# Kernel optimization log

Measured on AMD Instinct MI355X. Metric: run time of the kernel, lower is better.

Reference implementation:

```python
import jax, jax.numpy as jnp
import numpy as np

B, T_DEC, F = 16, 32, 8
S_ENC, H, L = 256, 512, 2
TGT_IDX = jnp.arange(8)  # target_indices = all features


def setup_inputs() -> dict:
    key = jax.random.key(0)
    ks = jax.random.split(key, 16)
    g = lambda k, shp, s=0.05: jax.random.normal(k, shp, dtype=jnp.float32) * s
    return {
        'target': jax.random.normal(ks[0], (B, T_DEC, F), dtype=jnp.float32),
        'hidden0': jax.random.normal(ks[1], (L, B, H), dtype=jnp.float32),
        'enc_outputs': jax.random.normal(ks[2], (B, S_ENC, H), dtype=jnp.float32),
        # Attention params
        'attn_W': g(ks[3], (H, 2 * H)), 'attn_b': jnp.zeros((H,), jnp.float32),
        'v_w': g(ks[4], (H,)),
        # GRU layer 0 (input = F + H) and layer 1 (input = H); PyTorch layout [3H, in]
        'gru_Wih0': g(ks[5], (3 * H, F + H)), 'gru_Whh0': g(ks[6], (3 * H, H)),
        'gru_bih0': jnp.zeros((3 * H,), jnp.float32), 'gru_bhh0': jnp.zeros((3 * H,), jnp.float32),
        'gru_Wih1': g(ks[7], (3 * H, H)), 'gru_Whh1': g(ks[8], (3 * H, H)),
        'gru_bih1': jnp.zeros((3 * H,), jnp.float32), 'gru_bhh1': jnp.zeros((3 * H,), jnp.float32),
        # output Linear (2H + F -> F)
        'out_W': g(ks[9], (F, 2 * H + F)), 'out_b': jnp.zeros((F,), jnp.float32),
        'input_seq_len': S_ENC,
    }


def _gru_cell(x, h, Wih, Whh, bih, bhh):
    # PyTorch GRUCell math; gate order [r, z, n]
    gi = x @ Wih.T + bih
    gh = h @ Whh.T + bhh
    ir, iz, inn = jnp.split(gi, 3, axis=-1)
    hr, hz, hn = jnp.split(gh, 3, axis=-1)
    r = jax.nn.sigmoid(ir + hr)
    z = jax.nn.sigmoid(iz + hz)
    n = jnp.tanh(inn + r * hn)
    return (1.0 - z) * n + z * h


def reference(target, hidden0, enc_outputs, attn_W, attn_b, v_w,
              gru_Wih0, gru_Whh0, gru_bih0, gru_bhh0,
              gru_Wih1, gru_Whh1, gru_bih1, gru_bhh1,
              out_W, out_b, input_seq_len):
    b, s, h = enc_outputs.shape

    def step(carry, target_t):
        hidden, x_in = carry  # hidden [L,B,H], x_in [B,F]
        h_top = hidden[-1]
        # Bahdanau attention
        hid_rep = jnp.broadcast_to(h_top[:, None, :], (b, s, h))
        energy = jnp.tanh(jnp.concatenate([hid_rep, enc_outputs], axis=-1) @ attn_W.T + attn_b)
        scores = energy @ v_w  # [B,S]
        weightings = jax.nn.softmax(scores, axis=1)
        weighted = jnp.einsum('bs,bsh->bh', weightings, enc_outputs)  # [B,H]
        # stacked GRU single step
        x = jnp.concatenate([x_in, weighted], axis=-1)  # [B, F+H]
        h0 = _gru_cell(x, hidden[0], gru_Wih0, gru_Whh0, gru_bih0, gru_bhh0)
        h1 = _gru_cell(h0, hidden[1], gru_Wih1, gru_Whh1, gru_bih1, gru_bhh1)
        new_hidden = jnp.stack([h0, h1])
        # output projection + relu (applied in DecoderBase.forward)
        out = jnp.concatenate([h1, weighted, x_in], axis=-1) @ out_W.T + out_b
        out = jax.nn.relu(out)  # [B,F]
        # no teacher forcing (teacher_force_prob=None): replace target features with prediction
        next_in = target_t.at[:, TGT_IDX].set(out)
        return (new_hidden, next_in), out

    target_ts = jnp.swapaxes(target, 0, 1)  # [T,B,F]
    (_, _), outs = jax.lax.scan(step, (hidden0, target[:, 0, :]), target_ts)
    return jnp.swapaxes(outs, 0, 1)  # [B,T,F]
```

## Files before the change

### kernel.cpp

```cpp
#include <hip/hip_runtime.h>


namespace {
constexpr int NBLK = 256, NTHR = 256;


constexpr int OFF_AEH   = 8192;
constexpr int OFF_WHID  = OFF_AEH + 131072;
constexpr int OFF_WIH0  = OFF_WHID + 131072;
constexpr int OFF_WHH0  = OFF_WIH0 + 399360;
constexpr int OFF_WIH1  = OFF_WHH0 + 393216;
constexpr int OFF_WHH1  = OFF_WIH1 + 393216;
constexpr int OFF_ENCP  = OFF_WHH1 + 393216;
constexpr int OFF_H0C   = OFF_ENCP + 1048576;
constexpr int OFF_H1C   = OFF_H0C + 4096;
constexpr int OFF_HIDPS = OFF_H1C + 4096;
constexpr int OFF_WPART = OFF_HIDPS + 8192;
constexpr int OFF_H0S   = OFF_WPART + 135168;
constexpr int OFF_H1S   = OFF_H0S + 4096;

constexpr int L_H1   = 0;
constexpr int L_H0   = 256;
constexpr int L_HIDP = 512;
constexpr int L_ES   = 1024;
constexpr int L_HX   = 1040;
constexpr int L_AX   = 1304;
constexpr int L_AH   = 1400;
constexpr int L_BIH0 = 1496, L_BHH0 = 1592, L_BIH1 = 1688, L_BHH1 = 1784;
constexpr int L_VW   = 1880;
constexpr int L_XINL = 2392;
constexpr int LDS_FLOATS = 8192;
}

typedef _Float16 h2 __attribute__((ext_vector_type(2)));
union U32H { unsigned u; h2 h; };

__device__ __forceinline__ float dot2(unsigned a, unsigned b, float acc) {
    U32H ua, ub; ua.u = a; ub.u = b;
#if __has_builtin(__builtin_amdgcn_fdot2)
    return __builtin_amdgcn_fdot2(ua.h, ub.h, acc, false);
#else
    return acc + (float)ua.h.x * (float)ub.h.x + (float)ua.h.y * (float)ub.h.y;
#endif
}
__device__ __forceinline__ unsigned packh2(float a, float b) {
    U32H u; u.h = h2{(_Float16)a, (_Float16)b}; return u.u;
}
__device__ __forceinline__ float fsig(float x) { return 1.0f / (1.0f + __expf(-x)); }
__device__ __forceinline__ float ftanhf(float x) {
    float e = __expf(2.0f * x);
    return 1.0f - 2.0f / (e + 1.0f);
}
__device__ __forceinline__ float cload(const float* p) {
    return __hip_atomic_load(p, __ATOMIC_RELAXED, __HIP_MEMORY_SCOPE_SYSTEM);
}
__device__ __forceinline__ void cstore(float* p, float v) {
    __hip_atomic_store(p, v, __ATOMIC_RELAXED, __HIP_MEMORY_SCOPE_SYSTEM);
}
__device__ __forceinline__ unsigned ucload(const unsigned* p) {
    return __hip_atomic_load(p, __ATOMIC_RELAXED, __HIP_MEMORY_SCOPE_SYSTEM);
}
__device__ __forceinline__ void ucstore(unsigned* p, unsigned v) {
    __hip_atomic_store(p, v, __ATOMIC_RELAXED, __HIP_MEMORY_SCOPE_SYSTEM);
}

__device__ __forceinline__ void bar_sync_flush(unsigned* cnt, unsigned target) {
    __syncthreads();
    if (threadIdx.x == 0) {
        __builtin_amdgcn_fence(__ATOMIC_RELEASE, "agent");
        __hip_atomic_fetch_add(cnt, 1u, __ATOMIC_RELAXED, __HIP_MEMORY_SCOPE_SYSTEM);
        while (__hip_atomic_load(cnt, __ATOMIC_RELAXED, __HIP_MEMORY_SCOPE_SYSTEM) < target)
            __builtin_amdgcn_s_sleep(8);
        __builtin_amdgcn_fence(__ATOMIC_ACQUIRE, "agent");
    }
    __syncthreads();
}

__global__ __launch_bounds__(NTHR) void decoder_kernel(
    const float* __restrict__ target, const float* __restrict__ hidden0,
    const float* __restrict__ enc, const float* __restrict__ attn_W,
    const float* __restrict__ attn_b, const float* __restrict__ v_w,
    const float* __restrict__ Wih0, const float* __restrict__ Whh0,
    const float* __restrict__ bih0, const float* __restrict__ bhh0,
    const float* __restrict__ Wih1, const float* __restrict__ Whh1,
    const float* __restrict__ bih1, const float* __restrict__ bhh1,
    const float* __restrict__ outW, const float* __restrict__ outBias,
    float* __restrict__ out, float* __restrict__ ws) {
    const int tid = threadIdx.x, bid = blockIdx.x;
    const int b = bid >> 4, s = bid & 15;
    unsigned* tags = (unsigned*)ws;
    unsigned* gridCnt = (unsigned*)ws + 8180;

    unsigned* aehU  = (unsigned*)(ws + OFF_AEH);
    unsigned* whidU = (unsigned*)(ws + OFF_WHID);
    unsigned* wih0U = (unsigned*)(ws + OFF_WIH0);
    unsigned* whh0U = (unsigned*)(ws + OFF_WHH0);
    unsigned* wih1U = (unsigned*)(ws + OFF_WIH1);
    unsigned* whh1U = (unsigned*)(ws + OFF_WHH1);
    unsigned* encpU = (unsigned*)(ws + OFF_ENCP);
    unsigned* h0cU = (unsigned*)(ws + OFF_H0C);
    unsigned* h1cU = (unsigned*)(ws + OFF_H1C);
    float* hidPS = ws + OFF_HIDPS;
    float* wpart = ws + OFF_WPART;
    unsigned* h0S = (unsigned*)(ws + OFF_H0S);
    unsigned* h1S = (unsigned*)(ws + OFF_H1S);

    __shared__ __align__(16) float lds[LDS_FLOATS];
    unsigned* ldsU = (unsigned*)lds;
    const int gtid = bid * NTHR + tid;

    for (int i = gtid; i < 131072; i += NBLK * NTHR) {
        const int jr = i >> 8, p = i & 255;
        aehU[i]  = packh2(attn_W[jr * 1024 + 512 + 2 * p], attn_W[jr * 1024 + 513 + 2 * p]);
        whidU[i] = packh2(attn_W[jr * 1024 + 2 * p], attn_W[jr * 1024 + 1 + 2 * p]);
    }
    for (int i = gtid; i < 399360; i += NBLK * NTHR)
        wih0U[i] = packh2(Wih0[2 * i], Wih0[2 * i + 1]);
    for (int i = gtid; i < 393216; i += NBLK * NTHR) {
        whh0U[i] = packh2(Whh0[2 * i], Whh0[2 * i + 1]);
        wih1U[i] = packh2(Wih1[2 * i], Wih1[2 * i + 1]);
        whh1U[i] = packh2(Whh1[2 * i], Whh1[2 * i + 1]);
    }
    if (gtid < 4096) {
        const int bb = gtid >> 8, p = gtid & 255;
        h0cU[gtid] = packh2(hidden0[bb * 512 + 2 * p], hidden0[bb * 512 + 2 * p + 1]);
        h1cU[gtid] = packh2(hidden0[8192 + bb * 512 + 2 * p], hidden0[8192 + bb * 512 + 2 * p + 1]);
    }
    bar_sync_flush(gridCnt, NBLK);

    {
        for (int i = 0; i < 32; ++i) {
            const int idx = tid + i * 256;
            lds[idx] = enc[(b * 256 + s * 16) * 512 + idx];
        }
        __syncthreads();
        float a0[16], a1[16];
        const float bb0 = attn_b[2 * tid], bb1 = attn_b[2 * tid + 1];
#pragma unroll
        for (int sl = 0; sl < 16; ++sl) { a0[sl] = bb0; a1[sl] = bb1; }
        const unsigned* w0 = &aehU[(2 * tid) * 256];
        const unsigned* w1 = &aehU[(2 * tid + 1) * 256];
        for (int p = 0; p < 256; ++p) {
            const unsigned ww0 = w0[p], ww1 = w1[p];
#pragma unroll
            for (int sl = 0; sl < 16; ++sl) {
                const unsigned epk = packh2(lds[sl * 512 + 2 * p], lds[sl * 512 + 2 * p + 1]);
                a0[sl] = dot2(epk, ww0, a0[sl]);
                a1[sl] = dot2(epk, ww1, a1[sl]);
            }
        }
        for (int sl = 0; sl < 16; ++sl)
            encpU[(b * 256 + s * 16 + sl) * 256 + tid] = packh2(a0[sl], a1[sl]);
        __syncthreads();
    }

    if (tid < 96) {
        const int grow = (tid >> 5) * 512 + s * 32 + (tid & 31);
        lds[L_BIH0 + tid] = bih0[grow]; lds[L_BHH0 + tid] = bhh0[grow];
        lds[L_BIH1 + tid] = bih1[grow]; lds[L_BHH1 + tid] = bhh1[grow];
    }
    lds[L_VW + tid] = v_w[tid];
    lds[L_VW + 256 + tid] = v_w[256 + tid];
    __syncthreads();

    ldsU[L_H1 + tid] = ucload(&h1cU[b * 256 + tid]);
    ldsU[L_H0 + tid] = ucload(&h0cU[b * 256 + tid]);
    if (tid < 8) lds[L_XINL + tid] = target[b * 256 + tid];
    __syncthreads();

    for (int t = 0; t < 32; ++t) {
        const unsigned tgt = (unsigned)(t + 1);

        {
            const int r = tid >> 3, sub = tid & 7;
            const uint4* wrow = (const uint4*)&whidU[(s * 32 + r) * 256 + sub * 32];
            const uint4* h1p = (const uint4*)&ldsU[L_H1 + sub * 32];
            float acc = 0.f;
#pragma unroll
            for (int k4 = 0; k4 < 8; ++k4) {
                const uint4 hv = h1p[k4], wv = wrow[k4];
                acc = dot2(hv.x, wv.x, acc); acc = dot2(hv.y, wv.y, acc);
                acc = dot2(hv.z, wv.z, acc); acc = dot2(hv.w, wv.w, acc);
            }
            acc += __shfl_down(acc, 4, 8); acc += __shfl_down(acc, 2, 8); acc += __shfl_down(acc, 1, 8);
            if (sub == 0) cstore(&hidPS[(b * 16 + s) * 32 + r], acc);
        }
        __syncthreads();
        if (tid == 0) ucstore(&tags[(b * 16 + s) * 32 + 0], tgt);
        {
            const unsigned* tg = &tags[(b * 16 + (tid & 15)) * 32 + 0];
            while (ucload(tg) < tgt) __builtin_amdgcn_s_sleep(1);
        }
        __builtin_amdgcn_fence(__ATOMIC_ACQUIRE, "workgroup");
        lds[L_HIDP + tid] = cload(&hidPS[(b * 16 + (tid >> 5)) * 32 + (tid & 31)]);
        lds[L_HIDP + 256 + tid] = cload(&hidPS[(b * 16 + 8 + (tid >> 5)) * 32 + (tid & 31)]);
        __syncthreads();

        {
            const int sloc = tid >> 4, sub = tid & 15;
            const unsigned* ep = &encpU[(b * 256 + s * 16 + sloc) * 256];
            float acc = 0.f;
#pragma unroll 4
            for (int k2 = 0; k2 < 16; ++k2) {
                const int p = k2 * 16 + sub;
                U32H u; u.u = ep[p];
                acc += lds[L_VW + 2 * p] * ftanhf((float)u.h.x + lds[L_HIDP + 2 * p]);
                acc += lds[L_VW + 2 * p + 1] * ftanhf((float)u.h.y + lds[L_HIDP + 2 * p + 1]);
            }
            acc += __shfl_down(acc, 8, 16); acc += __shfl_down(acc, 4, 16);
            acc += __shfl_down(acc, 2, 16); acc += __shfl_down(acc, 1, 16);
            if (sub == 0) lds[L_ES + sloc] = __expf(acc);
        }
        __syncthreads();
        {
            float wp0 = 0.f, wp1 = 0.f;
            const float2* er = (const float2*)&enc[(b * 256 + s * 16) * 512];
#pragma unroll
            for (int sl = 0; sl < 16; ++sl) {
                const float2 e = er[sl * 256 + tid];
                const float es = lds[L_ES + sl];
                wp0 += es * e.x; wp1 += es * e.y;
            }
            cstore(&wpart[(b * 16 + s) * 528 + 2 * tid], wp0);
            cstore(&wpart[(b * 16 + s) * 528 + 2 * tid + 1], wp1);
            if (tid == 0) {
                float l = 0.f;
#pragma unroll
                for (int i = 0; i < 16; ++i) l += lds[L_ES + i];
                cstore(&wpart[(b * 16 + s) * 528 + 512], l);
            }
        }
        __syncthreads();
        if (tid == 0) ucstore(&tags[(b * 16 + s) * 32 + 1], tgt);
        {
            const unsigned* tg = &tags[(b * 16 + (tid & 15)) * 32 + 1];
            while (ucload(tg) < tgt) __builtin_amdgcn_s_sleep(1);
        }
        __builtin_amdgcn_fence(__ATOMIC_ACQUIRE, "workgroup");
        {
            float w0 = 0.f, w1 = 0.f;
#pragma unroll
            for (int sp = 0; sp < 16; ++sp) {
                w0 += cload(&wpart[(b * 16 + sp) * 528 + 2 * tid]);
                w1 += cload(&wpart[(b * 16 + sp) * 528 + 2 * tid + 1]);
            }
            if (tid < 16) lds[L_ES + tid] = cload(&wpart[(b * 16 + tid) * 528 + 512]);
            __syncthreads();
            float L = 0.f;
#pragma unroll
            for (int i = 0; i < 16; ++i) L += lds[L_ES + i];
            const float inv = 1.f / L;
            ldsU[L_HX + 4 + tid] = packh2(w0 * inv, w1 * inv);
            if (tid < 4) {
                ldsU[L_HX + tid] = packh2(lds[L_XINL + 2 * tid], lds[L_XINL + 2 * tid + 1]);
                ldsU[L_HX + 260 + tid] = 0u;
            }
        }
        __syncthreads();

        if (tid < 192) {
            const int u = tid >> 1, sub = tid & 1;
            const int gh = u >> 5, r = u & 31;
            const int grow = gh * 512 + s * 32 + r;
            const uint4* wx = (const uint4*)&wih0U[grow * 260 + sub * 132];
            const uint4* xp = (const uint4*)&ldsU[L_HX + sub * 132];
            float ax = 0.f;
#pragma unroll 11
            for (int k4 = 0; k4 < 33; ++k4) {
                const uint4 xv = xp[k4], wv = wx[k4];
                ax = dot2(xv.x, wv.x, ax); ax = dot2(xv.y, wv.y, ax);
                ax = dot2(xv.z, wv.z, ax); ax = dot2(xv.w, wv.w, ax);
            }
            const uint4* wh = (const uint4*)&whh0U[grow * 256 + sub * 128];
            const uint4* hp = (const uint4*)&ldsU[L_H0 + sub * 128];
            float ah = 0.f;
#pragma unroll 8
            for (int k4 = 0; k4 < 32; ++k4) {
                const uint4 hv = hp[k4], wv = wh[k4];
                ah = dot2(hv.x, wv.x, ah); ah = dot2(hv.y, wv.y, ah);
                ah = dot2(hv.z, wv.z, ah); ah = dot2(hv.w, wv.w, ah);
            }
            ax += __shfl_down(ax, 1, 2); ah += __shfl_down(ah, 1, 2);
            if (sub == 0) {
                lds[L_AX + u] = ax + lds[L_BIH0 + u];
                lds[L_AH + u] = ah + lds[L_BHH0 + u];
            }
        }
        __syncthreads();
        if (tid < 32) {
            const int r = tid;
            const float rg = fsig(lds[L_AX + r] + lds[L_AH + r]);
            const float z = fsig(lds[L_AX + 32 + r] + lds[L_AH + 32 + r]);
            const float n = ftanhf(lds[L_AX + 64 + r] + rg * lds[L_AH + 64 + r]);
            U32H u; u.u = ldsU[L_H0 + s * 16 + (r >> 1)];
            const float hold = (r & 1) ? (float)u.h.y : (float)u.h.x;
            const float hs = (1.f - z) * n + z * hold;
            const float hsn = __shfl_down(hs, 1, 2);
            if ((r & 1) == 0)
                ucstore(&h0S[(b * 16 + s) * 16 + (r >> 1)], packh2(hs, hsn));
        }
        __syncthreads();
        if (tid == 0) ucstore(&tags[(b * 16 + s) * 32 + 2], tgt);
        {
            const unsigned* tg = &tags[(b * 16 + (tid & 15)) * 32 + 2];
            while (ucload(tg) < tgt) __builtin_amdgcn_s_sleep(1);
        }
        __builtin_amdgcn_fence(__ATOMIC_ACQUIRE, "workgroup");
        ldsU[L_H0 + tid] = ucload(&h0S[(b * 16 + (tid >> 4)) * 16 + (tid & 15)]);
        __syncthreads();

        if (tid < 192) {
            const int u = tid >> 1, sub = tid & 1;
            const int gh = u >> 5, r = u & 31;
            const int grow = gh * 512 + s * 32 + r;
            const uint4* wx = (const uint4*)&wih1U[grow * 256 + sub * 128];
            const uint4* xp = (const uint4*)&ldsU[L_H0 + sub * 128];
            float ax = 0.f;
#pragma unroll 8
            for (int k4 = 0; k4 < 32; ++k4) {
                const uint4 xv = xp[k4], wv = wx[k4];
                ax = dot2(xv.x, wv.x, ax); ax = dot2(xv.y, wv.y, ax);
                ax = dot2(xv.z, wv.z, ax); ax = dot2(xv.w, wv.w, ax);
            }
            const uint4* wh = (const uint4*)&whh1U[grow * 256 + sub * 128];
            const uint4* hp = (const uint4*)&ldsU[L_H1 + sub * 128];
            float ah = 0.f;
#pragma unroll 8
            for (int k4 = 0; k4 < 32; ++k4) {
                const uint4 hv = hp[k4], wv = wh[k4];
                ah = dot2(hv.x, wv.x, ah); ah = dot2(hv.y, wv.y, ah);
                ah = dot2(hv.z, wv.z, ah); ah = dot2(hv.w, wv.w, ah);
            }
            ax += __shfl_down(ax, 1, 2); ah += __shfl_down(ah, 1, 2);
            if (sub == 0) {
                lds[L_AX + u] = ax + lds[L_BIH1 + u];
                lds[L_AH + u] = ah + lds[L_BHH1 + u];
            }
        }
        __syncthreads();
        if (tid < 32) {
            const int r = tid;
            const float rg = fsig(lds[L_AX + r] + lds[L_AH + r]);
            const float z = fsig(lds[L_AX + 32 + r] + lds[L_AH + 32 + r]);
            const float n = ftanhf(lds[L_AX + 64 + r] + rg * lds[L_AH + 64 + r]);
            U32H u; u.u = ldsU[L_H1 + s * 16 + (r >> 1)];
            const float hold = (r & 1) ? (float)u.h.y : (float)u.h.x;
            const float hs = (1.f - z) * n + z * hold;
            const float hsn = __shfl_down(hs, 1, 2);
            if ((r & 1) == 0)
                ucstore(&h1S[(b * 16 + s) * 16 + (r >> 1)], packh2(hs, hsn));
        }
        __syncthreads();
        if (tid == 0) ucstore(&tags[(b * 16 + s) * 32 + 3], tgt);
        {
            const unsigned* tg = &tags[(b * 16 + (tid & 15)) * 32 + 3];
            while (ucload(tg) < tgt) __builtin_amdgcn_s_sleep(1);
        }
        __builtin_amdgcn_fence(__ATOMIC_ACQUIRE, "workgroup");
        ldsU[L_H1 + tid] = ucload(&h1S[(b * 16 + (tid >> 4)) * 16 + (tid & 15)]);
        __syncthreads();

        {
            const int f = tid >> 5, l = tid & 31;
            const float* ow = &outW[f * 1032];
            float acc = 0.f;
#pragma unroll
            for (int i = 0; i < 8; ++i) {
                const int k2 = i * 32 + l;
                U32H u; u.u = ldsU[L_H1 + k2];
                acc += ow[2 * k2] * (float)u.h.x + ow[2 * k2 + 1] * (float)u.h.y;
            }
#pragma unroll
            for (int i = 0; i < 8; ++i) {
                const int k2 = i * 32 + l;
                U32H u; u.u = ldsU[L_HX + 4 + k2];
                acc += ow[512 + 2 * k2] * (float)u.h.x + ow[512 + 2 * k2 + 1] * (float)u.h.y;
            }
            if (l < 8) acc += ow[1024 + l] * lds[L_XINL + l];
            acc += __shfl_down(acc, 16, 32); acc += __shfl_down(acc, 8, 32);
            acc += __shfl_down(acc, 4, 32); acc += __shfl_down(acc, 2, 32);
            acc += __shfl_down(acc, 1, 32);
            if (l == 0) {
                const float o = fmaxf(acc + outBias[f], 0.f);
                lds[L_ES + f] = o;
                if (s == 0) out[b * 256 + t * 8 + f] = o;
            }
        }
        __syncthreads();
        if (tid < 8) lds[L_XINL + tid] = lds[L_ES + tid];
        __syncthreads();
    }
}

extern "C" void kernel_launch(void* const* d_in, const int* in_sizes, int n_in,
                              void* d_out, int out_size, void* d_ws, size_t ws_size,
                              hipStream_t stream) {
    (void)in_sizes; (void)n_in; (void)out_size; (void)ws_size;
    hipMemsetAsync(d_ws, 0, 32768, stream);
    decoder_kernel<<<NBLK, NTHR, 0, stream>>>(
        (const float*)d_in[0], (const float*)d_in[1], (const float*)d_in[2],
        (const float*)d_in[3], (const float*)d_in[4], (const float*)d_in[5],
        (const float*)d_in[6], (const float*)d_in[7], (const float*)d_in[8],
        (const float*)d_in[9], (const float*)d_in[10], (const float*)d_in[11],
        (const float*)d_in[12], (const float*)d_in[13], (const float*)d_in[14],
        (const float*)d_in[15], (float*)d_out, (float*)d_ws);
}
```

Measured before the change: 896.0 us.

## Split prologue into separate kernels and use stamped LL messages for inter-block exchange

Moves the weight packing and encoder projection into separate kernel launches, which removes the in-kernel grid barrier and reduces the decoder's LDS footprint. Three of the four per-step flag-then-data exchanges between the 16 blocks of a batch row are replaced by 64-bit stores that carry the payload together with a step stamp, so consumers poll the data directly instead of waiting on a separate tag. The attention partial exchange still uses a flag, but now one wave signals per 64 threads after a vmcnt wait rather than going through a block-wide barrier. This trades extra launches and a larger memset for fewer barrier round trips on the serial 32-step critical path, and it relies on the inline-asm sc0/sc1 coherence being correct.

Measured after the change: 1.040 ms. +16.0%, slower.

```diff
diff --git a/kernel.cpp b/kernel.cpp
--- a/kernel.cpp
+++ b/kernel.cpp
@@ -2,22 +2,21 @@
 
 
 namespace {
-constexpr int NBLK = 256, NTHR = 256;
-
-
-constexpr int OFF_AEH   = 8192;
-constexpr int OFF_WHID  = OFF_AEH + 131072;
-constexpr int OFF_WIH0  = OFF_WHID + 131072;
-constexpr int OFF_WHH0  = OFF_WIH0 + 399360;
-constexpr int OFF_WIH1  = OFF_WHH0 + 393216;
-constexpr int OFF_WHH1  = OFF_WIH1 + 393216;
-constexpr int OFF_ENCP  = OFF_WHH1 + 393216;
-constexpr int OFF_H0C   = OFF_ENCP + 1048576;
-constexpr int OFF_H1C   = OFF_H0C + 4096;
-constexpr int OFF_HIDPS = OFF_H1C + 4096;
-constexpr int OFF_WPART = OFF_HIDPS + 8192;
-constexpr int OFF_H0S   = OFF_WPART + 135168;
-constexpr int OFF_H1S   = OFF_H0S + 4096;
+constexpr int NTHR_P = 256, NBLK_P = 256;
+constexpr int NTHR = 256, NBLK = 256;
+
+constexpr int OFF_FLG     = 0;
+constexpr int OFF_HIDP_LL = 4096;
+constexpr int OFF_H0LL    = 20480;
+constexpr int OFF_H1LL    = 28672;
+constexpr int OFF_ATTP    = 36864;
+constexpr int OFF_AEH     = 168448;
+constexpr int OFF_WHID    = OFF_AEH + 131072;
+constexpr int OFF_WIH0    = OFF_WHID + 131072;
+constexpr int OFF_WHH0    = OFF_WIH0 + 399360;
+constexpr int OFF_WIH1    = OFF_WHH0 + 393216;
+constexpr int OFF_WHH1    = OFF_WIH1 + 393216;
+constexpr int OFF_ENCP    = OFF_WHH1 + 393216;
 
 constexpr int L_H1   = 0;
 constexpr int L_H0   = 256;
@@ -26,10 +25,11 @@
 constexpr int L_HX   = 1040;
 constexpr int L_AX   = 1304;
 constexpr int L_AH   = 1400;
-constexpr int L_BIH0 = 1496, L_BHH0 = 1592, L_BIH1 = 1688, L_BHH1 = 1784;
-constexpr int L_VW   = 1880;
-constexpr int L_XINL = 2392;
-constexpr int LDS_FLOATS = 8192;
+constexpr int L_HS   = 1496;
+constexpr int L_BIH0 = 1528, L_BHH0 = 1624, L_BIH1 = 1720, L_BHH1 = 1816;
+constexpr int L_VW   = 1912;
+constexpr int L_XIN  = 2424;
+constexpr int LDS_FLOATS = 2432;
 }
 
 typedef _Float16 h2 __attribute__((ext_vector_type(2)));
@@ -60,99 +60,110 @@
 __device__ __forceinline__ unsigned ucload(const unsigned* p) {
     return __hip_atomic_load(p, __ATOMIC_RELAXED, __HIP_MEMORY_SCOPE_SYSTEM);
 }
-__device__ __forceinline__ void ucstore(unsigned* p, unsigned v) {
-    __hip_atomic_store(p, v, __ATOMIC_RELAXED, __HIP_MEMORY_SCOPE_SYSTEM);
-}
-
-__device__ __forceinline__ void bar_sync_flush(unsigned* cnt, unsigned target) {
-    __syncthreads();
-    if (threadIdx.x == 0) {
-        __builtin_amdgcn_fence(__ATOMIC_RELEASE, "agent");
-        __hip_atomic_fetch_add(cnt, 1u, __ATOMIC_RELAXED, __HIP_MEMORY_SCOPE_SYSTEM);
-        while (__hip_atomic_load(cnt, __ATOMIC_RELAXED, __HIP_MEMORY_SCOPE_SYSTEM) < target)
-            __builtin_amdgcn_s_sleep(8);
-        __builtin_amdgcn_fence(__ATOMIC_ACQUIRE, "agent");
-    }
-    __syncthreads();
-}
-
-__global__ __launch_bounds__(NTHR) void decoder_kernel(
-    const float* __restrict__ target, const float* __restrict__ hidden0,
-    const float* __restrict__ enc, const float* __restrict__ attn_W,
-    const float* __restrict__ attn_b, const float* __restrict__ v_w,
-    const float* __restrict__ Wih0, const float* __restrict__ Whh0,
-    const float* __restrict__ bih0, const float* __restrict__ bhh0,
-    const float* __restrict__ Wih1, const float* __restrict__ Whh1,
-    const float* __restrict__ bih1, const float* __restrict__ bhh1,
-    const float* __restrict__ outW, const float* __restrict__ outBias,
-    float* __restrict__ out, float* __restrict__ ws) {
-    const int tid = threadIdx.x, bid = blockIdx.x;
-    const int b = bid >> 4, s = bid & 15;
-    unsigned* tags = (unsigned*)ws;
-    unsigned* gridCnt = (unsigned*)ws + 8180;
-
+
+__device__ __forceinline__ void ll_store(unsigned long long* p, unsigned payload,
+                                         unsigned stamp) {
+    unsigned long long v = (unsigned long long)payload | ((unsigned long long)stamp << 32);
+    asm volatile("global_store_dwordx2 %0, %1, off sc0 sc1" :: "v"(p), "v"(v) : "memory");
+}
+__device__ __forceinline__ unsigned long long ll_load(const unsigned long long* p) {
+    unsigned long long v;
+    asm volatile("global_load_dwordx2 %0, %1, off sc0 sc1\n\ts_waitcnt vmcnt(0)"
+                 : "=v"(v) : "v"(p) : "memory");
+    return v;
+}
+__device__ __forceinline__ unsigned ll_poll(const unsigned long long* p, unsigned stamp) {
+    for (;;) {
+        unsigned long long v = ll_load(p);
+        if ((unsigned)(v >> 32) == stamp) return (unsigned)v;
+        __builtin_amdgcn_s_sleep(1);
+    }
+}
+__device__ __forceinline__ void flag_store(unsigned* p, unsigned v) {
+    asm volatile("global_store_dword %0, %1, off sc0 sc1" :: "v"(p), "v"(v) : "memory");
+}
+
+__global__ __launch_bounds__(NTHR_P) void pack_kernel(
+    const float* __restrict__ attn_W, const float* __restrict__ Wih0,
+    const float* __restrict__ Whh0, const float* __restrict__ Wih1,
+    const float* __restrict__ Whh1, float* __restrict__ ws) {
     unsigned* aehU  = (unsigned*)(ws + OFF_AEH);
     unsigned* whidU = (unsigned*)(ws + OFF_WHID);
     unsigned* wih0U = (unsigned*)(ws + OFF_WIH0);
     unsigned* whh0U = (unsigned*)(ws + OFF_WHH0);
     unsigned* wih1U = (unsigned*)(ws + OFF_WIH1);
     unsigned* whh1U = (unsigned*)(ws + OFF_WHH1);
-    unsigned* encpU = (unsigned*)(ws + OFF_ENCP);
-    unsigned* h0cU = (unsigned*)(ws + OFF_H0C);
-    unsigned* h1cU = (unsigned*)(ws + OFF_H1C);
-    float* hidPS = ws + OFF_HIDPS;
-    float* wpart = ws + OFF_WPART;
-    unsigned* h0S = (unsigned*)(ws + OFF_H0S);
-    unsigned* h1S = (unsigned*)(ws + OFF_H1S);
-
-    __shared__ __align__(16) float lds[LDS_FLOATS];
-    unsigned* ldsU = (unsigned*)lds;
-    const int gtid = bid * NTHR + tid;
-
-    for (int i = gtid; i < 131072; i += NBLK * NTHR) {
+    const int gtid = blockIdx.x * NTHR_P + threadIdx.x;
+    for (int i = gtid; i < 131072; i += NBLK_P * NTHR_P) {
         const int jr = i >> 8, p = i & 255;
         aehU[i]  = packh2(attn_W[jr * 1024 + 512 + 2 * p], attn_W[jr * 1024 + 513 + 2 * p]);
         whidU[i] = packh2(attn_W[jr * 1024 + 2 * p], attn_W[jr * 1024 + 1 + 2 * p]);
     }
-    for (int i = gtid; i < 399360; i += NBLK * NTHR)
+    for (int i = gtid; i < 399360; i += NBLK_P * NTHR_P)
         wih0U[i] = packh2(Wih0[2 * i], Wih0[2 * i + 1]);
-    for (int i = gtid; i < 393216; i += NBLK * NTHR) {
+    for (int i = gtid; i < 393216; i += NBLK_P * NTHR_P) {
         whh0U[i] = packh2(Whh0[2 * i], Whh0[2 * i + 1]);
         wih1U[i] = packh2(Wih1[2 * i], Wih1[2 * i + 1]);
         whh1U[i] = packh2(Whh1[2 * i], Whh1[2 * i + 1]);
     }
-    if (gtid < 4096) {
-        const int bb = gtid >> 8, p = gtid & 255;
-        h0cU[gtid] = packh2(hidden0[bb * 512 + 2 * p], hidden0[bb * 512 + 2 * p + 1]);
-        h1cU[gtid] = packh2(hidden0[8192 + bb * 512 + 2 * p], hidden0[8192 + bb * 512 + 2 * p + 1]);
-    }
-    bar_sync_flush(gridCnt, NBLK);
-
-    {
-        for (int i = 0; i < 32; ++i) {
-            const int idx = tid + i * 256;
-            lds[idx] = enc[(b * 256 + s * 16) * 512 + idx];
-        }
-        __syncthreads();
-        float a0[16], a1[16];
-        const float bb0 = attn_b[2 * tid], bb1 = attn_b[2 * tid + 1];
-#pragma unroll
-        for (int sl = 0; sl < 16; ++sl) { a0[sl] = bb0; a1[sl] = bb1; }
-        const unsigned* w0 = &aehU[(2 * tid) * 256];
-        const unsigned* w1 = &aehU[(2 * tid + 1) * 256];
-        for (int p = 0; p < 256; ++p) {
-            const unsigned ww0 = w0[p], ww1 = w1[p];
-#pragma unroll
-            for (int sl = 0; sl < 16; ++sl) {
-                const unsigned epk = packh2(lds[sl * 512 + 2 * p], lds[sl * 512 + 2 * p + 1]);
-                a0[sl] = dot2(epk, ww0, a0[sl]);
-                a1[sl] = dot2(epk, ww1, a1[sl]);
-            }
-        }
-        for (int sl = 0; sl < 16; ++sl)
-            encpU[(b * 256 + s * 16 + sl) * 256 + tid] = packh2(a0[sl], a1[sl]);
-        __syncthreads();
-    }
+}
+
+__global__ __launch_bounds__(NTHR_P) void encp_kernel(
+    const float* __restrict__ enc, const float* __restrict__ attn_b,
+    float* __restrict__ ws) {
+    const int tid = threadIdx.x, bid = blockIdx.x;
+    const int b = bid >> 4, s = bid & 15;
+    const unsigned* aehU = (const unsigned*)(ws + OFF_AEH);
+    unsigned* encpU = (unsigned*)(ws + OFF_ENCP);
+    __shared__ __align__(16) float lds[8192];
+    for (int i = 0; i < 32; ++i) {
+        const int idx = tid + i * 256;
+        lds[idx] = enc[(b * 256 + s * 16) * 512 + idx];
+    }
+    __syncthreads();
+    float a0[16], a1[16];
+    const float bb0 = attn_b[2 * tid], bb1 = attn_b[2 * tid + 1];
+#pragma unroll
+    for (int sl = 0; sl < 16; ++sl) { a0[sl] = bb0; a1[sl] = bb1; }
+    const unsigned* w0 = &aehU[(2 * tid) * 256];
+    const unsigned* w1 = &aehU[(2 * tid + 1) * 256];
+    for (int p = 0; p < 256; ++p) {
+        const unsigned ww0 = w0[p], ww1 = w1[p];
+#pragma unroll
+        for (int sl = 0; sl < 16; ++sl) {
+            const unsigned epk = packh2(lds[sl * 512 + 2 * p], lds[sl * 512 + 2 * p + 1]);
+            a0[sl] = dot2(epk, ww0, a0[sl]);
+            a1[sl] = dot2(epk, ww1, a1[sl]);
+        }
+    }
+    for (int sl = 0; sl < 16; ++sl)
+        encpU[(b * 256 + s * 16 + sl) * 256 + tid] = packh2(a0[sl], a1[sl]);
+}
+
+__global__ __launch_bounds__(NTHR) void decoder_kernel(
+    const float* __restrict__ target, const float* __restrict__ hidden0,
+    const float* __restrict__ enc, const float* __restrict__ v_w,
+    const float* __restrict__ bih0, const float* __restrict__ bhh0,
+    const float* __restrict__ bih1, const float* __restrict__ bhh1,
+    const float* __restrict__ outW, const float* __restrict__ outBias,
+    float* __restrict__ out, float* __restrict__ ws) {
+    const int tid = threadIdx.x, bid = blockIdx.x;
+    const int b = bid >> 4, s = bid & 15;
+
+    unsigned* flg = (unsigned*)ws + OFF_FLG;
+    unsigned long long* hidpLL = (unsigned long long*)(ws + OFF_HIDP_LL);
+    unsigned long long* h0LL = (unsigned long long*)(ws + OFF_H0LL);
+    unsigned long long* h1LL = (unsigned long long*)(ws + OFF_H1LL);
+    float* attP = ws + OFF_ATTP;
+    const unsigned* whidU = (const unsigned*)(ws + OFF_WHID);
+    const unsigned* wih0U = (const unsigned*)(ws + OFF_WIH0);
+    const unsigned* whh0U = (const unsigned*)(ws + OFF_WHH0);
+    const unsigned* wih1U = (const unsigned*)(ws + OFF_WIH1);
+    const unsigned* whh1U = (const unsigned*)(ws + OFF_WHH1);
+    const unsigned* encpU = (const unsigned*)(ws + OFF_ENCP);
+
+    __shared__ __align__(16) float lds[LDS_FLOATS];
+    unsigned* ldsU = (unsigned*)lds;
 
     if (tid < 96) {
         const int grow = (tid >> 5) * 512 + s * 32 + (tid & 31);
@@ -161,11 +172,11 @@
     }
     lds[L_VW + tid] = v_w[tid];
     lds[L_VW + 256 + tid] = v_w[256 + tid];
-    __syncthreads();
-
-    ldsU[L_H1 + tid] = ucload(&h1cU[b * 256 + tid]);
-    ldsU[L_H0 + tid] = ucload(&h0cU[b * 256 + tid]);
-    if (tid < 8) lds[L_XINL + tid] = target[b * 256 + tid];
+    ldsU[L_H0 + tid] = packh2(hidden0[b * 512 + 2 * tid], hidden0[b * 512 + 2 * tid + 1]);
+    ldsU[L_H1 + tid] = packh2(hidden0[8192 + b * 512 + 2 * tid],
+                              hidden0[8192 + b * 512 + 2 * tid + 1]);
+    if (tid < 8) lds[L_XIN + tid] = target[b * 256 + tid];
+    if (tid < 4) ldsU[L_HX + 260 + tid] = 0u;
     __syncthreads();
 
     for (int t = 0; t < 32; ++t) {
@@ -183,17 +194,10 @@
                 acc = dot2(hv.z, wv.z, acc); acc = dot2(hv.w, wv.w, acc);
             }
             acc += __shfl_down(acc, 4, 8); acc += __shfl_down(acc, 2, 8); acc += __shfl_down(acc, 1, 8);
-            if (sub == 0) cstore(&hidPS[(b * 16 + s) * 32 + r], acc);
-        }
-        __syncthreads();
-        if (tid == 0) ucstore(&tags[(b * 16 + s) * 32 + 0], tgt);
-        {
-            const unsigned* tg = &tags[(b * 16 + (tid & 15)) * 32 + 0];
-            while (ucload(tg) < tgt) __builtin_amdgcn_s_sleep(1);
-        }
-        __builtin_amdgcn_fence(__ATOMIC_ACQUIRE, "workgroup");
-        lds[L_HIDP + tid] = cload(&hidPS[(b * 16 + (tid >> 5)) * 32 + (tid & 31)]);
-        lds[L_HIDP + 256 + tid] = cload(&hidPS[(b * 16 + 8 + (tid >> 5)) * 32 + (tid & 31)]);
+            if (sub == 0) ll_store(&hidpLL[b * 512 + s * 32 + r], __float_as_uint(acc), tgt);
+        }
+        lds[L_HIDP + tid] = __uint_as_float(ll_poll(&hidpLL[b * 512 + tid], tgt));
+        lds[L_HIDP + 256 + tid] = __uint_as_float(ll_poll(&hidpLL[b * 512 + 256 + tid], tgt));
         __syncthreads();
 
         {
@@ -221,30 +225,32 @@
                 const float es = lds[L_ES + sl];
                 wp0 += es * e.x; wp1 += es * e.y;
             }
-            cstore(&wpart[(b * 16 + s) * 528 + 2 * tid], wp0);
-            cstore(&wpart[(b * 16 + s) * 528 + 2 * tid + 1], wp1);
+            cstore(&attP[(b * 16 + s) * 514 + 2 * tid], wp0);
+            cstore(&attP[(b * 16 + s) * 514 + 2 * tid + 1], wp1);
             if (tid == 0) {
                 float l = 0.f;
 #pragma unroll
                 for (int i = 0; i < 16; ++i) l += lds[L_ES + i];
-                cstore(&wpart[(b * 16 + s) * 528 + 512], l);
-            }
-        }
-        __syncthreads();
-        if (tid == 0) ucstore(&tags[(b * 16 + s) * 32 + 1], tgt);
-        {
-            const unsigned* tg = &tags[(b * 16 + (tid & 15)) * 32 + 1];
-            while (ucload(tg) < tgt) __builtin_amdgcn_s_sleep(1);
-        }
+                cstore(&attP[(b * 16 + s) * 514 + 512], l);
+            }
+        }
+        asm volatile("s_waitcnt vmcnt(0)" ::: "memory");
+        if ((tid & 63) == 0)
+            flag_store(&flg[(b * 16 + s) * 16 + (tid >> 6) * 4], tgt);
+
+        if (tid < 64) {
+            const unsigned* fp = &flg[(b * 16 + (tid >> 2)) * 16 + (tid & 3) * 4];
+            while (ucload(fp) < tgt) __builtin_amdgcn_s_sleep(1);
+        }
+        __syncthreads();
         __builtin_amdgcn_fence(__ATOMIC_ACQUIRE, "workgroup");
         {
             float w0 = 0.f, w1 = 0.f;
-#pragma unroll
             for (int sp = 0; sp < 16; ++sp) {
-                w0 += cload(&wpart[(b * 16 + sp) * 528 + 2 * tid]);
-                w1 += cload(&wpart[(b * 16 + sp) * 528 + 2 * tid + 1]);
-            }
-            if (tid < 16) lds[L_ES + tid] = cload(&wpart[(b * 16 + tid) * 528 + 512]);
+                w0 += cload(&attP[(b * 16 + sp) * 514 + 2 * tid]);
+                w1 += cload(&attP[(b * 16 + sp) * 514 + 2 * tid + 1]);
+            }
+            if (tid < 16) lds[L_ES + tid] = cload(&attP[(b * 16 + tid) * 514 + 512]);
             __syncthreads();
             float L = 0.f;
 #pragma unroll
@@ -252,8 +258,7 @@
             const float inv = 1.f / L;
             ldsU[L_HX + 4 + tid] = packh2(w0 * inv, w1 * inv);
             if (tid < 4) {
-                ldsU[L_HX + tid] = packh2(lds[L_XINL + 2 * tid], lds[L_XINL + 2 * tid + 1]);
-                ldsU[L_HX + 260 + tid] = 0u;
+                ldsU[L_HX + tid] = packh2(lds[L_XIN + 2 * tid], lds[L_XIN + 2 * tid + 1]);
             }
         }
         __syncthreads();
@@ -294,19 +299,16 @@
             const float n = ftanhf(lds[L_AX + 64 + r] + rg * lds[L_AH + 64 + r]);
             U32H u; u.u = ldsU[L_H0 + s * 16 + (r >> 1)];
             const float hold = (r & 1) ? (float)u.h.y : (float)u.h.x;
-            const float hs = (1.f - z) * n + z * hold;
-            const float hsn = __shfl_down(hs, 1, 2);
-            if ((r & 1) == 0)
-                ucstore(&h0S[(b * 16 + s) * 16 + (r >> 1)], packh2(hs, hsn));
-        }
-        __syncthreads();
-        if (tid == 0) ucstore(&tags[(b * 16 + s) * 32 + 2], tgt);
-        {
-            const unsigned* tg = &tags[(b * 16 + (tid & 15)) * 32 + 2];
-            while (ucload(tg) < tgt) __builtin_amdgcn_s_sleep(1);
-        }
-        __builtin_amdgcn_fence(__ATOMIC_ACQUIRE, "workgroup");
-        ldsU[L_H0 + tid] = ucload(&h0S[(b * 16 + (tid >> 4)) * 16 + (tid & 15)]);
+            lds[L_HS + r] = (1.f - z) * n + z * hold;
+        }
+        __syncthreads();
+        if (tid < 16)
+            ll_store(&h0LL[(b * 16 + s) * 16 + tid],
+                     packh2(lds[L_HS + 2 * tid], lds[L_HS + 2 * tid + 1]), tgt);
+        {
+            const int sp = tid >> 4, jj = tid & 15;
+            ldsU[L_H0 + sp * 16 + jj] = ll_poll(&h0LL[(b * 16 + sp) * 16 + jj], tgt);
+        }
         __syncthreads();
 
         if (tid < 192) {
@@ -345,19 +347,16 @@
             const float n = ftanhf(lds[L_AX + 64 + r] + rg * lds[L_AH + 64 + r]);
             U32H u; u.u = ldsU[L_H1 + s * 16 + (r >> 1)];
             const float hold = (r & 1) ? (float)u.h.y : (float)u.h.x;
-            const float hs = (1.f - z) * n + z * hold;
-            const float hsn = __shfl_down(hs, 1, 2);
-            if ((r & 1) == 0)
-                ucstore(&h1S[(b * 16 + s) * 16 + (r >> 1)], packh2(hs, hsn));
-        }
-        __syncthreads();
-        if (tid == 0) ucstore(&tags[(b * 16 + s) * 32 + 3], tgt);
-        {
-            const unsigned* tg = &tags[(b * 16 + (tid & 15)) * 32 + 3];
-            while (ucload(tg) < tgt) __builtin_amdgcn_s_sleep(1);
-        }
-        __builtin_amdgcn_fence(__ATOMIC_ACQUIRE, "workgroup");
-        ldsU[L_H1 + tid] = ucload(&h1S[(b * 16 + (tid >> 4)) * 16 + (tid & 15)]);
+            lds[L_HS + r] = (1.f - z) * n + z * hold;
+        }
+        __syncthreads();
+        if (tid < 16)
+            ll_store(&h1LL[(b * 16 + s) * 16 + tid],
+                     packh2(lds[L_HS + 2 * tid], lds[L_HS + 2 * tid + 1]), tgt);
+        {
+            const int sp = tid >> 4, jj = tid & 15;
+            ldsU[L_H1 + sp * 16 + jj] = ll_poll(&h1LL[(b * 16 + sp) * 16 + jj], tgt);
+        }
         __syncthreads();
 
         {
@@ -376,7 +375,7 @@
                 U32H u; u.u = ldsU[L_HX + 4 + k2];
                 acc += ow[512 + 2 * k2] * (float)u.h.x + ow[512 + 2 * k2 + 1] * (float)u.h.y;
             }
-            if (l < 8) acc += ow[1024 + l] * lds[L_XINL + l];
+            if (l < 8) acc += ow[1024 + l] * lds[L_XIN + l];
             acc += __shfl_down(acc, 16, 32); acc += __shfl_down(acc, 8, 32);
             acc += __shfl_down(acc, 4, 32); acc += __shfl_down(acc, 2, 32);
             acc += __shfl_down(acc, 1, 32);
@@ -387,7 +386,7 @@
             }
         }
         __syncthreads();
-        if (tid < 8) lds[L_XINL + tid] = lds[L_ES + tid];
+        if (tid < 8) lds[L_XIN + tid] = lds[L_ES + tid];
         __syncthreads();
     }
 }
@@ -396,12 +395,15 @@
                               void* d_out, int out_size, void* d_ws, size_t ws_size,
                               hipStream_t stream) {
     (void)in_sizes; (void)n_in; (void)out_size; (void)ws_size;
-    hipMemsetAsync(d_ws, 0, 32768, stream);
+    hipMemsetAsync(d_ws, 0, 147456, stream);
+    pack_kernel<<<NBLK_P, NTHR_P, 0, stream>>>(
+        (const float*)d_in[3], (const float*)d_in[6], (const float*)d_in[7],
+        (const float*)d_in[10], (const float*)d_in[11], (float*)d_ws);
+    encp_kernel<<<NBLK_P, NTHR_P, 0, stream>>>(
+        (const float*)d_in[2], (const float*)d_in[4], (float*)d_ws);
     decoder_kernel<<<NBLK, NTHR, 0, stream>>>(
         (const float*)d_in[0], (const float*)d_in[1], (const float*)d_in[2],
-        (const float*)d_in[3], (const float*)d_in[4], (const float*)d_in[5],
-        (const float*)d_in[6], (const float*)d_in[7], (const float*)d_in[8],
-        (const float*)d_in[9], (const float*)d_in[10], (const float*)d_in[11],
+        (const float*)d_in[5], (const float*)d_in[8], (const float*)d_in[9],
         (const float*)d_in[12], (const float*)d_in[13], (const float*)d_in[14],
         (const float*)d_in[15], (float*)d_out, (float*)d_ws);
 }
```

## Poll flags with one wave, exchange normalized fp16 attention partials, drop hidden staging

Applied to the files above, without the earlier changes.

Tag polling now runs only in the first 16 threads followed by a workgroup barrier, instead of every thread spinning on global flags. Each block's attention-weighted partial sum is normalized locally and stored as packed fp16 together with its softmax denominator, so the cross-block gather reads half the bytes. The combine step then rescales by each block's denominator. The initial hidden state is packed straight from the input instead of through a staged global copy, and the workspace layout is compacted. This reduces global polling traffic and exchange bandwidth per timestep, at the cost of extra fp16 rounding of the partial context vectors and an added barrier per sync point.

Result: no change. 882.1 us (-1.6%).

```diff
diff --git a/kernel.cpp b/kernel.cpp
--- a/kernel.cpp
+++ b/kernel.cpp
@@ -2,22 +2,20 @@
 
 
 namespace {
-constexpr int NBLK = 256, NTHR = 256;
-
-
-constexpr int OFF_AEH   = 8192;
+constexpr int NTHR = 256, NBLK = 256;
+
+constexpr int OFF_HIDPS = 8192;
+constexpr int OFF_WNS   = 16384;
+constexpr int OFF_LS    = 81920;
+constexpr int OFF_H0S   = 82176;
+constexpr int OFF_H1S   = 86272;
+constexpr int OFF_AEH   = 90368;
 constexpr int OFF_WHID  = OFF_AEH + 131072;
 constexpr int OFF_WIH0  = OFF_WHID + 131072;
 constexpr int OFF_WHH0  = OFF_WIH0 + 399360;
 constexpr int OFF_WIH1  = OFF_WHH0 + 393216;
 constexpr int OFF_WHH1  = OFF_WIH1 + 393216;
 constexpr int OFF_ENCP  = OFF_WHH1 + 393216;
-constexpr int OFF_H0C   = OFF_ENCP + 1048576;
-constexpr int OFF_H1C   = OFF_H0C + 4096;
-constexpr int OFF_HIDPS = OFF_H1C + 4096;
-constexpr int OFF_WPART = OFF_HIDPS + 8192;
-constexpr int OFF_H0S   = OFF_WPART + 135168;
-constexpr int OFF_H1S   = OFF_H0S + 4096;
 
 constexpr int L_H1   = 0;
 constexpr int L_H0   = 256;
@@ -29,6 +27,7 @@
 constexpr int L_BIH0 = 1496, L_BHH0 = 1592, L_BIH1 = 1688, L_BHH1 = 1784;
 constexpr int L_VW   = 1880;
 constexpr int L_XINL = 2392;
+constexpr int L_LL   = 2400;
 constexpr int LDS_FLOATS = 8192;
 }
 
@@ -91,6 +90,11 @@
     unsigned* tags = (unsigned*)ws;
     unsigned* gridCnt = (unsigned*)ws + 8180;
 
+    float* hidPS = ws + OFF_HIDPS;
+    unsigned* wnS = (unsigned*)(ws + OFF_WNS);
+    float* lS = ws + OFF_LS;
+    unsigned* h0S = (unsigned*)(ws + OFF_H0S);
+    unsigned* h1S = (unsigned*)(ws + OFF_H1S);
     unsigned* aehU  = (unsigned*)(ws + OFF_AEH);
     unsigned* whidU = (unsigned*)(ws + OFF_WHID);
     unsigned* wih0U = (unsigned*)(ws + OFF_WIH0);
@@ -98,12 +102,6 @@
     unsigned* wih1U = (unsigned*)(ws + OFF_WIH1);
     unsigned* whh1U = (unsigned*)(ws + OFF_WHH1);
     unsigned* encpU = (unsigned*)(ws + OFF_ENCP);
-    unsigned* h0cU = (unsigned*)(ws + OFF_H0C);
-    unsigned* h1cU = (unsigned*)(ws + OFF_H1C);
-    float* hidPS = ws + OFF_HIDPS;
-    float* wpart = ws + OFF_WPART;
-    unsigned* h0S = (unsigned*)(ws + OFF_H0S);
-    unsigned* h1S = (unsigned*)(ws + OFF_H1S);
 
     __shared__ __align__(16) float lds[LDS_FLOATS];
     unsigned* ldsU = (unsigned*)lds;
@@ -121,11 +119,6 @@
         wih1U[i] = packh2(Wih1[2 * i], Wih1[2 * i + 1]);
         whh1U[i] = packh2(Whh1[2 * i], Whh1[2 * i + 1]);
     }
-    if (gtid < 4096) {
-        const int bb = gtid >> 8, p = gtid & 255;
-        h0cU[gtid] = packh2(hidden0[bb * 512 + 2 * p], hidden0[bb * 512 + 2 * p + 1]);
-        h1cU[gtid] = packh2(hidden0[8192 + bb * 512 + 2 * p], hidden0[8192 + bb * 512 + 2 * p + 1]);
-    }
     bar_sync_flush(gridCnt, NBLK);
 
     {
@@ -163,9 +156,11 @@
     lds[L_VW + 256 + tid] = v_w[256 + tid];
     __syncthreads();
 
-    ldsU[L_H1 + tid] = ucload(&h1cU[b * 256 + tid]);
-    ldsU[L_H0 + tid] = ucload(&h0cU[b * 256 + tid]);
+    ldsU[L_H1 + tid] = packh2(hidden0[8192 + b * 512 + 2 * tid],
+                              hidden0[8192 + b * 512 + 2 * tid + 1]);
+    ldsU[L_H0 + tid] = packh2(hidden0[b * 512 + 2 * tid], hidden0[b * 512 + 2 * tid + 1]);
     if (tid < 8) lds[L_XINL + tid] = target[b * 256 + tid];
+    if (tid < 4) ldsU[L_HX + 260 + tid] = 0u;
     __syncthreads();
 
     for (int t = 0; t < 32; ++t) {
@@ -187,10 +182,11 @@
         }
         __syncthreads();
         if (tid == 0) ucstore(&tags[(b * 16 + s) * 32 + 0], tgt);
-        {
-            const unsigned* tg = &tags[(b * 16 + (tid & 15)) * 32 + 0];
+        if (tid < 16) {
+            const unsigned* tg = &tags[(b * 16 + tid) * 32 + 0];
             while (ucload(tg) < tgt) __builtin_amdgcn_s_sleep(1);
         }
+        __syncthreads();
         __builtin_amdgcn_fence(__ATOMIC_ACQUIRE, "workgroup");
         lds[L_HIDP + tid] = cload(&hidPS[(b * 16 + (tid >> 5)) * 32 + (tid & 31)]);
         lds[L_HIDP + 256 + tid] = cload(&hidPS[(b * 16 + 8 + (tid >> 5)) * 32 + (tid & 31)]);
@@ -213,6 +209,10 @@
         }
         __syncthreads();
         {
+            float l = 0.f;
+#pragma unroll
+            for (int i = 0; i < 16; ++i) l += lds[L_ES + i];
+            const float invl = 1.f / l;
             float wp0 = 0.f, wp1 = 0.f;
             const float2* er = (const float2*)&enc[(b * 256 + s * 16) * 512];
 #pragma unroll
@@ -221,40 +221,33 @@
                 const float es = lds[L_ES + sl];
                 wp0 += es * e.x; wp1 += es * e.y;
             }
-            cstore(&wpart[(b * 16 + s) * 528 + 2 * tid], wp0);
-            cstore(&wpart[(b * 16 + s) * 528 + 2 * tid + 1], wp1);
-            if (tid == 0) {
-                float l = 0.f;
-#pragma unroll
-                for (int i = 0; i < 16; ++i) l += lds[L_ES + i];
-                cstore(&wpart[(b * 16 + s) * 528 + 512], l);
-            }
+            ucstore(&wnS[(b * 16 + s) * 256 + tid], packh2(wp0 * invl, wp1 * invl));
+            if (tid == 0) cstore(&lS[b * 16 + s], l);
         }
         __syncthreads();
         if (tid == 0) ucstore(&tags[(b * 16 + s) * 32 + 1], tgt);
-        {
-            const unsigned* tg = &tags[(b * 16 + (tid & 15)) * 32 + 1];
+        if (tid < 16) {
+            const unsigned* tg = &tags[(b * 16 + tid) * 32 + 1];
             while (ucload(tg) < tgt) __builtin_amdgcn_s_sleep(1);
-        }
+            lds[L_LL + tid] = cload(&lS[b * 16 + tid]);
+        }
+        __syncthreads();
         __builtin_amdgcn_fence(__ATOMIC_ACQUIRE, "workgroup");
         {
+            float Lsum = 0.f;
+#pragma unroll
+            for (int i = 0; i < 16; ++i) Lsum += lds[L_LL + i];
+            const float inv = 1.f / Lsum;
             float w0 = 0.f, w1 = 0.f;
 #pragma unroll
             for (int sp = 0; sp < 16; ++sp) {
-                w0 += cload(&wpart[(b * 16 + sp) * 528 + 2 * tid]);
-                w1 += cload(&wpart[(b * 16 + sp) * 528 + 2 * tid + 1]);
-            }
-            if (tid < 16) lds[L_ES + tid] = cload(&wpart[(b * 16 + tid) * 528 + 512]);
-            __syncthreads();
-            float L = 0.f;
-#pragma unroll
-            for (int i = 0; i < 16; ++i) L += lds[L_ES + i];
-            const float inv = 1.f / L;
+                U32H u; u.u = ucload(&wnS[(b * 16 + sp) * 256 + tid]);
+                const float Ls = lds[L_LL + sp];
+                w0 += Ls * (float)u.h.x; w1 += Ls * (float)u.h.y;
+            }
             ldsU[L_HX + 4 + tid] = packh2(w0 * inv, w1 * inv);
-            if (tid < 4) {
+            if (tid < 4)
                 ldsU[L_HX + tid] = packh2(lds[L_XINL + 2 * tid], lds[L_XINL + 2 * tid + 1]);
-                ldsU[L_HX + 260 + tid] = 0u;
-            }
         }
         __syncthreads();
 
@@ -301,10 +294,11 @@
         }
         __syncthreads();
         if (tid == 0) ucstore(&tags[(b * 16 + s) * 32 + 2], tgt);
-        {
-            const unsigned* tg = &tags[(b * 16 + (tid & 15)) * 32 + 2];
+        if (tid < 16) {
+            const unsigned* tg = &tags[(b * 16 + tid) * 32 + 2];
             while (ucload(tg) < tgt) __builtin_amdgcn_s_sleep(1);
         }
+        __syncthreads();
         __builtin_amdgcn_fence(__ATOMIC_ACQUIRE, "workgroup");
         ldsU[L_H0 + tid] = ucload(&h0S[(b * 16 + (tid >> 4)) * 16 + (tid & 15)]);
         __syncthreads();
@@ -352,10 +346,11 @@
         }
         __syncthreads();
         if (tid == 0) ucstore(&tags[(b * 16 + s) * 32 + 3], tgt);
-        {
-            const unsigned* tg = &tags[(b * 16 + (tid & 15)) * 32 + 3];
+        if (tid < 16) {
+            const unsigned* tg = &tags[(b * 16 + tid) * 32 + 3];
             while (ucload(tg) < tgt) __builtin_amdgcn_s_sleep(1);
         }
+        __syncthreads();
         __builtin_amdgcn_fence(__ATOMIC_ACQUIRE, "workgroup");
         ldsU[L_H1 + tid] = ucload(&h1S[(b * 16 + (tid >> 4)) * 16 + (tid & 15)]);
         __syncthreads();
```
